# Kernel tuning notes

Measured on AMD Instinct MI355X. Metric: run time of the kernel, lower is better.

The kernel has to match this reference:

```python
import jax, jax.numpy as jnp
import numpy as np

EPS = 1e-08
NUM_EMBEDDINGS = 8192
EMBEDDING_DIM = 256
N_TOKENS = 32768


def setup_inputs() -> dict:
    key = jax.random.key(0)
    k1, k2, k3 = jax.random.split(key, 3)
    input_data = jax.random.normal(k1, (N_TOKENS, EMBEDDING_DIM), dtype=jnp.float32)
    rand = jax.random.normal(k2, (N_TOKENS, EMBEDDING_DIM), dtype=jnp.float32)
    codebooks = jax.random.normal(k3, (NUM_EMBEDDINGS, EMBEDDING_DIM), dtype=jnp.float32)
    return {"input_data": input_data, "rand": rand, "codebooks": codebooks}


def reference(input_data, rand, codebooks):
    # d2: (N, K) -- this full matrix is what a fused kernel would avoid.
    d2 = (jnp.sum(input_data * input_data, axis=1, keepdims=True)
          - 2.0 * input_data @ codebooks.T
          + jnp.sum(codebooks * codebooks, axis=1)[None, :])
    min_idx = jnp.argmin(d2, axis=1)                      # (N,)
    hard_q = codebooks[min_idx]                           # (N, D)

    # Noise substitution: scale unit-ish gaussian noise to the residual norm.
    r_norm = jnp.linalg.norm(input_data - hard_q, axis=1, keepdims=True)
    n_norm = jnp.linalg.norm(rand, axis=1, keepdims=True)
    quantized_input = input_data + (r_norm / (n_norm + EPS)) * rand

    # Perplexity from codebook usage counts (no grad path in original).
    counts = jnp.zeros((NUM_EMBEDDINGS,), dtype=jnp.float32).at[min_idx].add(1.0)
    total = jnp.maximum(counts.sum(), 1.0)
    avg_probs = counts / total
    perplexity = jnp.exp(-jnp.sum(avg_probs * jnp.log(avg_probs + EPS)))
    num_unique_indices = jnp.sum(counts > 0).astype(jnp.int32)
    return quantized_input, perplexity, num_unique_indices
```

## Files before the change

### kernel.cpp

```cpp
#include <hip/hip_runtime.h>
#include <stdint.h>

#define N_TOKENS 32768
#define N_CODES  8192
#define DIM      256
#define EPSF     1e-8f

typedef __bf16 bf16x8 __attribute__((ext_vector_type(8)));
typedef float  f32x4  __attribute__((ext_vector_type(4)));
typedef unsigned short ushort8 __attribute__((ext_vector_type(8)));

#define WS_CNORM_OFF  (4u*1024u*1024u)
#define WS_HIST_OFF   (WS_CNORM_OFF + N_CODES*4u)

__global__ __launch_bounds__(256) void k_prep(const float* __restrict__ cbf,
                                              unsigned short* __restrict__ cbh,
                                              float* __restrict__ cnorm,
                                              int* __restrict__ hist) {
    const int g   = blockIdx.x;
    const int tid = threadIdx.x;
    if (g < 32) hist[g * 256 + tid] = 0;

    __shared__ float nrm[16];
    if (tid < 16) nrm[tid] = 0.f;
    __syncthreads();

    #pragma unroll
    for (int i = 0; i < 2; ++i) {
        const int e  = i * 256 + tid;
        const int kc = e >> 6;
        const int ln = e & 63;
        const int lq = ln >> 4, lr = ln & 15;
        const float* src = cbf + ((size_t)(g * 16 + lr)) * DIM + kc * 32 + lq * 8;
        const float4 v0 = ((const float4*)src)[0];
        const float4 v1 = ((const float4*)src)[1];

        ushort8 u;
        u[0] = __builtin_bit_cast(unsigned short, (__bf16)v0.x);
        u[1] = __builtin_bit_cast(unsigned short, (__bf16)v0.y);
        u[2] = __builtin_bit_cast(unsigned short, (__bf16)v0.z);
        u[3] = __builtin_bit_cast(unsigned short, (__bf16)v0.w);
        u[4] = __builtin_bit_cast(unsigned short, (__bf16)v1.x);
        u[5] = __builtin_bit_cast(unsigned short, (__bf16)v1.y);
        u[6] = __builtin_bit_cast(unsigned short, (__bf16)v1.z);
        u[7] = __builtin_bit_cast(unsigned short, (__bf16)v1.w);
        *(ushort8*)((char*)cbh + (size_t)g * 8192 + kc * 1024 + ln * 16) = u;

        const float p = v0.x*v0.x + v0.y*v0.y + v0.z*v0.z + v0.w*v0.w
                      + v1.x*v1.x + v1.y*v1.y + v1.z*v1.z + v1.w*v1.w;
        atomicAdd(&nrm[lr], p);
    }
    __syncthreads();
    if (tid < 16) cnorm[g * 16 + tid] = nrm[tid];
}

__global__ __launch_bounds__(512, 2) void k_argmin(const float* __restrict__ X,
                                                   const float* __restrict__ R,
                                                   const unsigned short* __restrict__ cbh,
                                                   const float* __restrict__ cnorm,
                                                   float* __restrict__ out,
                                                   int* __restrict__ hist) {
    __shared__ __attribute__((aligned(16))) char smem[74240];
    float* redv  = (float*)(smem + 69632);
    int*   redi  = (int*)(smem + 71680);
    float* maxvS = (float*)(smem + 73728);

    const int tid  = threadIdx.x;
    const int w    = tid >> 6;
    const int lane = tid & 63;
    const int lr   = lane & 15;
    const int lq   = lane >> 4;
    const int th   = w >> 2;
    const int wc   = w & 3;
    const int r0   = blockIdx.x * 128;
    const int mycol = wc * 16 + lr;

    {
        const float4* Xf4 = (const float4*)(X + (size_t)(r0 + 16 * w) * DIM);
        #pragma unroll
        for (int i = 0; i < 16; ++i) {
            const float4 v = Xf4[i * 64 + lane];
            ushort4 u;
            u.x = __builtin_bit_cast(unsigned short, (__bf16)v.x);
            u.y = __builtin_bit_cast(unsigned short, (__bf16)v.y);
            u.z = __builtin_bit_cast(unsigned short, (__bf16)v.z);
            u.w = __builtin_bit_cast(unsigned short, (__bf16)v.w);
            *(ushort4*)(smem + (16 * w + i) * 544 + lane * 8) = u;
        }
    }
    __syncthreads();

    bf16x8 A[4][8];
    #pragma unroll
    for (int mf = 0; mf < 4; ++mf)
        #pragma unroll
        for (int kc = 0; kc < 8; ++kc)
            A[mf][kc] = *(const bf16x8*)(smem + (64 * th + mf * 16 + lr) * 544 + kc * 64 + lq * 16);

    float maxv[16];
    int   maxi[16];
    #pragma unroll
    for (int i = 0; i < 16; ++i) { maxv[i] = -3.4e38f; maxi[i] = 0; }

    const unsigned int voff  = (unsigned int)(wc * 8192 + lane * 16);
    const unsigned int voff2 = voff + 4096u;
    const unsigned int voffc = (unsigned int)(mycol * 4);

    bf16x8 bA[8], bB[8];
    float cnA, cnB;

#define ISSUE_GRP(buf, cnv, chunk) do {                                               \
    const unsigned short* gb_ = (const unsigned short*)((const char*)cbh +            \
                                                        (size_t)(chunk) * 32768);    \
    const float* cb_ = cnorm + (size_t)(chunk) * 64;                                  \
    asm volatile("global_load_dwordx4 %0, %1, %2"             : "=v"(buf[0]) : "v"(voff),  "s"(gb_)); \
    asm volatile("global_load_dwordx4 %0, %1, %2 offset:1024" : "=v"(buf[1]) : "v"(voff),  "s"(gb_)); \
    asm volatile("global_load_dwordx4 %0, %1, %2 offset:2048" : "=v"(buf[2]) : "v"(voff),  "s"(gb_)); \
    asm volatile("global_load_dwordx4 %0, %1, %2 offset:3072" : "=v"(buf[3]) : "v"(voff),  "s"(gb_)); \
    asm volatile("global_load_dwordx4 %0, %1, %2"             : "=v"(buf[4]) : "v"(voff2), "s"(gb_)); \
    asm volatile("global_load_dwordx4 %0, %1, %2 offset:1024" : "=v"(buf[5]) : "v"(voff2), "s"(gb_)); \
    asm volatile("global_load_dwordx4 %0, %1, %2 offset:2048" : "=v"(buf[6]) : "v"(voff2), "s"(gb_)); \
    asm volatile("global_load_dwordx4 %0, %1, %2 offset:3072" : "=v"(buf[7]) : "v"(voff2), "s"(gb_)); \
    asm volatile("global_load_dword %0, %1, %2"               : "=v"(cnv)    : "v"(voffc), "s"(cb_)); \
} while (0)

#define WAITV9 do { asm volatile("s_waitcnt vmcnt(9)" ::: "memory");                  \
                    __builtin_amdgcn_sched_barrier(0); } while (0)
#define WAITV0 do { asm volatile("s_waitcnt vmcnt(0)" ::: "memory");                  \
                    __builtin_amdgcn_sched_barrier(0); } while (0)

#define COMPUTE_CHUNK(chunk, buf, cnv) do {                                           \
    f32x4 acc_[4];                                                                    \
    _Pragma("unroll") for (int mf_ = 0; mf_ < 4; ++mf_) {                             \
        acc_[mf_][0] = 0.f; acc_[mf_][1] = 0.f; acc_[mf_][2] = 0.f; acc_[mf_][3] = 0.f; } \
    _Pragma("unroll") for (int kc_ = 0; kc_ < 8; ++kc_)                               \
        _Pragma("unroll") for (int mf_ = 0; mf_ < 4; ++mf_)                           \
            acc_[mf_] = __builtin_amdgcn_mfma_f32_16x16x32_bf16(A[mf_][kc_], buf[kc_],\
                                                                acc_[mf_], 0, 0, 0);  \
    const int col_ = (chunk) * 64 + mycol;                                            \
    _Pragma("unroll") for (int mf_ = 0; mf_ < 4; ++mf_)                               \
        _Pragma("unroll") for (int r_ = 0; r_ < 4; ++r_) {                            \
            const float v_ = fmaf(-0.5f, (cnv), acc_[mf_][r_]);                       \
            const int j_ = mf_ * 4 + r_;                                              \
            if (v_ > maxv[j_]) { maxv[j_] = v_; maxi[j_] = col_; }                    \
        }                                                                             \
} while (0)

    ISSUE_GRP(bA, cnA, 0);
    ISSUE_GRP(bB, cnB, 1);

    for (int cc = 0; cc < 126; cc += 2) {
        WAITV9;
        COMPUTE_CHUNK(cc, bA, cnA);
        ISSUE_GRP(bA, cnA, cc + 2);
        WAITV9;
        COMPUTE_CHUNK(cc + 1, bB, cnB);
        ISSUE_GRP(bB, cnB, cc + 3);
    }
    WAITV9;
    COMPUTE_CHUNK(126, bA, cnA);
    WAITV0;
    COMPUTE_CHUNK(127, bB, cnB);

#undef ISSUE_GRP
#undef WAITV9
#undef WAITV0
#undef COMPUTE_CHUNK

    #pragma unroll
    for (int mf = 0; mf < 4; ++mf)
        #pragma unroll
        for (int r = 0; r < 4; ++r) {
            float v = maxv[mf * 4 + r]; int ix = maxi[mf * 4 + r];
            #pragma unroll
            for (int d = 1; d <= 8; d <<= 1) {
                const float ov = __shfl_xor(v, d);
                const int   oi = __shfl_xor(ix, d);
                if (ov > v || (ov == v && oi < ix)) { v = ov; ix = oi; }
            }
            if (lr == 0) {
                const int row = mf * 16 + lq * 4 + r;
                redv[w * 64 + row] = v; redi[w * 64 + row] = ix;
            }
        }
    __syncthreads();

    if (tid < 128) {
        const int t = tid, tth = t >> 6, tl = t & 63;
        float v = redv[(4 * tth) * 64 + tl]; int ix = redi[(4 * tth) * 64 + tl];
        #pragma unroll
        for (int ww = 1; ww < 4; ++ww) {
            const float ov = redv[(4 * tth + ww) * 64 + tl];
            const int   oi = redi[(4 * tth + ww) * 64 + tl];
            if (ov > v || (ov == v && oi < ix)) { v = ov; ix = oi; }
        }
        maxvS[t] = v;
        atomicAdd(&hist[ix], 1);
    }
    __syncthreads();

    for (int i = 0; i < 16; ++i) {
        const int tl = 16 * w + i;
        const int tok = r0 + tl;
        const float4 x = ((const float4*)(X + (size_t)tok * DIM))[lane];
        const float4 r = ((const float4*)(R + (size_t)tok * DIM))[lane];

        float x2 = x.x * x.x + x.y * x.y + x.z * x.z + x.w * x.w;
        float n2 = r.x * r.x + r.y * r.y + r.z * r.z + r.w * r.w;
        #pragma unroll
        for (int d = 1; d < 64; d <<= 1) {
            x2 += __shfl_xor(x2, d);
            n2 += __shfl_xor(n2, d);
        }
        const float mv = maxvS[tl];
        const float d2 = fmaxf(fmaf(-2.f, mv, x2), 0.f);
        const float s = sqrtf(d2) / (sqrtf(n2) + EPSF);

        float4 o;
        o.x = fmaf(s, r.x, x.x);
        o.y = fmaf(s, r.y, x.y);
        o.z = fmaf(s, r.z, x.z);
        o.w = fmaf(s, r.w, x.w);
        ((float4*)(out + (size_t)tok * DIM))[lane] = o;
    }
}

__global__ __launch_bounds__(1024) void k_stats(const int* __restrict__ hist,
                                                float* __restrict__ outs) {
    float s = 0.f; int u = 0;
    for (int b = threadIdx.x; b < N_CODES; b += 1024) {
        const float c = (float)hist[b];
        if (c > 0.f) ++u;
        const float p = c * (1.f / (float)N_TOKENS);
        s += p * logf(p + EPSF);
    }
    #pragma unroll
    for (int d = 1; d < 64; d <<= 1) {
        s += __shfl_xor(s, d);
        u += __shfl_xor(u, d);
    }
    __shared__ float ss[16];
    __shared__ int   su[16];
    const int w = threadIdx.x >> 6, lane = threadIdx.x & 63;
    if (lane == 0) { ss[w] = s; su[w] = u; }
    __syncthreads();
    if (threadIdx.x == 0) {
        float st = 0.f; int ut = 0;
        #pragma unroll
        for (int i = 0; i < 16; ++i) { st += ss[i]; ut += su[i]; }
        outs[0] = expf(-st);
        outs[1] = (float)ut;
    }
}

extern "C" void kernel_launch(void* const* d_in, const int* in_sizes, int n_in,
                              void* d_out, int out_size, void* d_ws, size_t ws_size,
                              hipStream_t stream) {
    const float* X = (const float*)d_in[0];
    const float* R = (const float*)d_in[1];
    const float* C = (const float*)d_in[2];
    float* out = (float*)d_out;

    char* ws = (char*)d_ws;
    unsigned short* cbh = (unsigned short*)ws;
    float* cnorm = (float*)(ws + WS_CNORM_OFF);
    int*   hist  = (int*)(ws + WS_HIST_OFF);

    k_prep  <<<512,            256, 0, stream>>>(C, cbh, cnorm, hist);
    k_argmin<<<N_TOKENS / 128, 512, 0, stream>>>(X, R, cbh, cnorm, out, hist);
    k_stats <<<1, 1024, 0, stream>>>(hist, out + (size_t)N_TOKENS * DIM);
}
```

Measured before the change: 233.8 us.

## Stage codebook norms in LDS, fuse stats into argmin, coalesce prep

Codebook norms are copied once per block into shared memory, replacing the per-chunk global norm load. The perplexity/unique-count kernel is folded into the argmin kernel through a last-block atomic counter, which removes a launch. Prep now reads codebook rows coalesced and reduces norms with wave shuffles, and the MFMA loop raises wave priority. The larger LDS footprint may prevent two blocks per CU.

```diff
diff --git a/kernel.cpp b/kernel.cpp
--- a/kernel.cpp
+++ b/kernel.cpp
@@ -13,45 +13,41 @@
 #define WS_CNORM_OFF  (4u*1024u*1024u)
 #define WS_HIST_OFF   (WS_CNORM_OFF + N_CODES*4u)
 
+__device__ int g_ctr;
+
 __global__ __launch_bounds__(256) void k_prep(const float* __restrict__ cbf,
                                               unsigned short* __restrict__ cbh,
                                               float* __restrict__ cnorm,
                                               int* __restrict__ hist) {
-    const int g   = blockIdx.x;
-    const int tid = threadIdx.x;
+    const int g    = blockIdx.x;
+    const int tid  = threadIdx.x;
+    const int w    = tid >> 6;
+    const int lane = tid & 63;
     if (g < 32) hist[g * 256 + tid] = 0;
-
-    __shared__ float nrm[16];
-    if (tid < 16) nrm[tid] = 0.f;
-    __syncthreads();
-
-    #pragma unroll
-    for (int i = 0; i < 2; ++i) {
-        const int e  = i * 256 + tid;
-        const int kc = e >> 6;
-        const int ln = e & 63;
-        const int lq = ln >> 4, lr = ln & 15;
-        const float* src = cbf + ((size_t)(g * 16 + lr)) * DIM + kc * 32 + lq * 8;
-        const float4 v0 = ((const float4*)src)[0];
-        const float4 v1 = ((const float4*)src)[1];
-
-        ushort8 u;
-        u[0] = __builtin_bit_cast(unsigned short, (__bf16)v0.x);
-        u[1] = __builtin_bit_cast(unsigned short, (__bf16)v0.y);
-        u[2] = __builtin_bit_cast(unsigned short, (__bf16)v0.z);
-        u[3] = __builtin_bit_cast(unsigned short, (__bf16)v0.w);
-        u[4] = __builtin_bit_cast(unsigned short, (__bf16)v1.x);
-        u[5] = __builtin_bit_cast(unsigned short, (__bf16)v1.y);
-        u[6] = __builtin_bit_cast(unsigned short, (__bf16)v1.z);
-        u[7] = __builtin_bit_cast(unsigned short, (__bf16)v1.w);
-        *(ushort8*)((char*)cbh + (size_t)g * 8192 + kc * 1024 + ln * 16) = u;
-
-        const float p = v0.x*v0.x + v0.y*v0.y + v0.z*v0.z + v0.w*v0.w
-                      + v1.x*v1.x + v1.y*v1.y + v1.z*v1.z + v1.w*v1.w;
-        atomicAdd(&nrm[lr], p);
-    }
-    __syncthreads();
-    if (tid < 16) cnorm[g * 16 + tid] = nrm[tid];
+    if (g == 0 && tid == 0) g_ctr = 0;
+
+    const int kc = lane >> 3;
+    const int lq = (lane >> 1) & 3;
+    const int jj = (lane & 1) * 4;
+
+    #pragma unroll
+    for (int i = 0; i < 4; ++i) {
+        const int row = 4 * w + i;
+        const float4 v = ((const float4*)(cbf + (size_t)(g * 16 + row) * DIM))[lane];
+
+        float sq = v.x * v.x + v.y * v.y + v.z * v.z + v.w * v.w;
+        #pragma unroll
+        for (int d = 1; d < 64; d <<= 1) sq += __shfl_xor(sq, d);
+        if (lane == 0) cnorm[g * 16 + row] = sq;
+
+        ushort4 u;
+        u.x = __builtin_bit_cast(unsigned short, (__bf16)v.x);
+        u.y = __builtin_bit_cast(unsigned short, (__bf16)v.y);
+        u.z = __builtin_bit_cast(unsigned short, (__bf16)v.z);
+        u.w = __builtin_bit_cast(unsigned short, (__bf16)v.w);
+        *(ushort4*)((char*)cbh + (size_t)g * 8192 + kc * 1024 +
+                    (lq * 16 + row) * 16 + jj * 2) = u;
+    }
 }
 
 __global__ __launch_bounds__(512, 2) void k_argmin(const float* __restrict__ X,
@@ -60,10 +56,12 @@
                                                    const float* __restrict__ cnorm,
                                                    float* __restrict__ out,
                                                    int* __restrict__ hist) {
-    __shared__ __attribute__((aligned(16))) char smem[74240];
+    __shared__ __attribute__((aligned(16))) char smem[107008];
+    __shared__ int amLast;
     float* redv  = (float*)(smem + 69632);
     int*   redi  = (int*)(smem + 71680);
     float* maxvS = (float*)(smem + 73728);
+    float* cnS   = (float*)(smem + 74240);
 
     const int tid  = threadIdx.x;
     const int w    = tid >> 6;
@@ -88,6 +86,12 @@
             *(ushort4*)(smem + (16 * w + i) * 544 + lane * 8) = u;
         }
     }
+    {
+        float4* dst = (float4*)cnS;
+        const float4* src = (const float4*)cnorm;
+        #pragma unroll
+        for (int i = 0; i < 4; ++i) dst[i * 512 + tid] = src[i * 512 + tid];
+    }
     __syncthreads();
 
     bf16x8 A[4][8];
@@ -104,15 +108,12 @@
 
     const unsigned int voff  = (unsigned int)(wc * 8192 + lane * 16);
     const unsigned int voff2 = voff + 4096u;
-    const unsigned int voffc = (unsigned int)(mycol * 4);
 
     bf16x8 bA[8], bB[8];
-    float cnA, cnB;
-
-#define ISSUE_GRP(buf, cnv, chunk) do {                                               \
+
+#define ISSUE_GRP(buf, chunk) do {                                                    \
     const unsigned short* gb_ = (const unsigned short*)((const char*)cbh +            \
                                                         (size_t)(chunk) * 32768);    \
-    const float* cb_ = cnorm + (size_t)(chunk) * 64;                                  \
     asm volatile("global_load_dwordx4 %0, %1, %2"             : "=v"(buf[0]) : "v"(voff),  "s"(gb_)); \
     asm volatile("global_load_dwordx4 %0, %1, %2 offset:1024" : "=v"(buf[1]) : "v"(voff),  "s"(gb_)); \
     asm volatile("global_load_dwordx4 %0, %1, %2 offset:2048" : "=v"(buf[2]) : "v"(voff),  "s"(gb_)); \
@@ -121,49 +122,51 @@
     asm volatile("global_load_dwordx4 %0, %1, %2 offset:1024" : "=v"(buf[5]) : "v"(voff2), "s"(gb_)); \
     asm volatile("global_load_dwordx4 %0, %1, %2 offset:2048" : "=v"(buf[6]) : "v"(voff2), "s"(gb_)); \
     asm volatile("global_load_dwordx4 %0, %1, %2 offset:3072" : "=v"(buf[7]) : "v"(voff2), "s"(gb_)); \
-    asm volatile("global_load_dword %0, %1, %2"               : "=v"(cnv)    : "v"(voffc), "s"(cb_)); \
 } while (0)
 
-#define WAITV9 do { asm volatile("s_waitcnt vmcnt(9)" ::: "memory");                  \
+#define WAITV8 do { asm volatile("s_waitcnt vmcnt(8)" ::: "memory");                  \
                     __builtin_amdgcn_sched_barrier(0); } while (0)
 #define WAITV0 do { asm volatile("s_waitcnt vmcnt(0)" ::: "memory");                  \
                     __builtin_amdgcn_sched_barrier(0); } while (0)
 
-#define COMPUTE_CHUNK(chunk, buf, cnv) do {                                           \
+#define COMPUTE_CHUNK(chunk, buf) do {                                                \
+    const float cn_ = cnS[(chunk) * 64 + mycol];                                      \
     f32x4 acc_[4];                                                                    \
     _Pragma("unroll") for (int mf_ = 0; mf_ < 4; ++mf_) {                             \
         acc_[mf_][0] = 0.f; acc_[mf_][1] = 0.f; acc_[mf_][2] = 0.f; acc_[mf_][3] = 0.f; } \
+    __builtin_amdgcn_s_setprio(1);                                                    \
     _Pragma("unroll") for (int kc_ = 0; kc_ < 8; ++kc_)                               \
         _Pragma("unroll") for (int mf_ = 0; mf_ < 4; ++mf_)                           \
             acc_[mf_] = __builtin_amdgcn_mfma_f32_16x16x32_bf16(A[mf_][kc_], buf[kc_],\
                                                                 acc_[mf_], 0, 0, 0);  \
+    __builtin_amdgcn_s_setprio(0);                                                    \
     const int col_ = (chunk) * 64 + mycol;                                            \
     _Pragma("unroll") for (int mf_ = 0; mf_ < 4; ++mf_)                               \
         _Pragma("unroll") for (int r_ = 0; r_ < 4; ++r_) {                            \
-            const float v_ = fmaf(-0.5f, (cnv), acc_[mf_][r_]);                       \
+            const float v_ = fmaf(-0.5f, cn_, acc_[mf_][r_]);                         \
             const int j_ = mf_ * 4 + r_;                                              \
             if (v_ > maxv[j_]) { maxv[j_] = v_; maxi[j_] = col_; }                    \
         }                                                                             \
 } while (0)
 
-    ISSUE_GRP(bA, cnA, 0);
-    ISSUE_GRP(bB, cnB, 1);
+    ISSUE_GRP(bA, 0);
+    ISSUE_GRP(bB, 1);
 
     for (int cc = 0; cc < 126; cc += 2) {
-        WAITV9;
-        COMPUTE_CHUNK(cc, bA, cnA);
-        ISSUE_GRP(bA, cnA, cc + 2);
-        WAITV9;
-        COMPUTE_CHUNK(cc + 1, bB, cnB);
-        ISSUE_GRP(bB, cnB, cc + 3);
-    }
-    WAITV9;
-    COMPUTE_CHUNK(126, bA, cnA);
+        WAITV8;
+        COMPUTE_CHUNK(cc, bA);
+        ISSUE_GRP(bA, cc + 2);
+        WAITV8;
+        COMPUTE_CHUNK(cc + 1, bB);
+        ISSUE_GRP(bB, cc + 3);
+    }
+    WAITV8;
+    COMPUTE_CHUNK(126, bA);
     WAITV0;
-    COMPUTE_CHUNK(127, bB, cnB);
+    COMPUTE_CHUNK(127, bB);
 
 #undef ISSUE_GRP
-#undef WAITV9
+#undef WAITV8
 #undef WAITV0
 #undef COMPUTE_CHUNK
 
@@ -223,33 +226,37 @@
         o.w = fmaf(s, r.w, x.w);
         ((float4*)(out + (size_t)tok * DIM))[lane] = o;
     }
-}
-
-__global__ __launch_bounds__(1024) void k_stats(const int* __restrict__ hist,
-                                                float* __restrict__ outs) {
-    float s = 0.f; int u = 0;
-    for (int b = threadIdx.x; b < N_CODES; b += 1024) {
-        const float c = (float)hist[b];
-        if (c > 0.f) ++u;
-        const float p = c * (1.f / (float)N_TOKENS);
-        s += p * logf(p + EPSF);
-    }
-    #pragma unroll
-    for (int d = 1; d < 64; d <<= 1) {
-        s += __shfl_xor(s, d);
-        u += __shfl_xor(u, d);
-    }
-    __shared__ float ss[16];
-    __shared__ int   su[16];
-    const int w = threadIdx.x >> 6, lane = threadIdx.x & 63;
-    if (lane == 0) { ss[w] = s; su[w] = u; }
-    __syncthreads();
-    if (threadIdx.x == 0) {
-        float st = 0.f; int ut = 0;
-        #pragma unroll
-        for (int i = 0; i < 16; ++i) { st += ss[i]; ut += su[i]; }
-        outs[0] = expf(-st);
-        outs[1] = (float)ut;
+
+    if (tid == 0) {
+        __threadfence();
+        amLast = (atomicAdd(&g_ctr, 1) == (int)gridDim.x - 1);
+    }
+    __syncthreads();
+    if (amLast) {
+        __threadfence();
+        float s = 0.f; int u = 0;
+        for (int b = tid; b < N_CODES; b += 512) {
+            const int c = __hip_atomic_load(&hist[b], __ATOMIC_RELAXED,
+                                            __HIP_MEMORY_SCOPE_AGENT);
+            if (c > 0) ++u;
+            const float p = (float)c * (1.f / (float)N_TOKENS);
+            s += p * logf(p + EPSF);
+        }
+        #pragma unroll
+        for (int d = 1; d < 64; d <<= 1) {
+            s += __shfl_xor(s, d);
+            u += __shfl_xor(u, d);
+        }
+        if (lane == 0) { redv[w] = s; redi[w] = u; }
+        __syncthreads();
+        if (tid == 0) {
+            float st = 0.f; int ut = 0;
+            #pragma unroll
+            for (int i = 0; i < 8; ++i) { st += redv[i]; ut += redi[i]; }
+            float* outs = out + (size_t)N_TOKENS * DIM;
+            outs[0] = expf(-st);
+            outs[1] = (float)ut;
+        }
     }
 }
 
@@ -268,5 +275,4 @@
 
     k_prep  <<<512,            256, 0, stream>>>(C, cbh, cnorm, hist);
     k_argmin<<<N_TOKENS / 128, 512, 0, stream>>>(X, R, cbh, cnorm, out, hist);
-    k_stats <<<1, 1024, 0, stream>>>(hist, out + (size_t)N_TOKENS * DIM);
 }
```

After: 251.5 us. +7.6%, slower.
